# Kernel optimization log

Hardware: AMD Instinct MI355X
Metric: run time of the kernel (lower is better)

## Reference

```python
import jax, jax.numpy as jnp
import numpy as np

B, T, S, H, E = 4, 2048, 2048, 16, 64  # batch, q_len, kv_len, heads, head_dim


def setup_inputs() -> dict:
    key = jax.random.key(0)
    kq, kk, kv, kl, kw = jax.random.split(key, 5)
    query = jax.random.normal(kq, (B, T, H * E), dtype=jnp.float32)
    key_t = jax.random.normal(kk, (B, S, H * E), dtype=jnp.float32)
    value = jax.random.normal(kv, (B, S, H * E), dtype=jnp.float32)
    # valid lengths in [S//2, S] so every row has at least one attendable key
    lengths = jax.random.randint(kl, (B,), S // 2, S + 1)
    key_padding_mask = jnp.arange(S)[None, :] < lengths[:, None]  # (B, S) bool, True = keep
    W_out = jax.random.normal(kw, (H * E, E), dtype=jnp.float32) * 0.02
    b_out = jnp.zeros((E,), dtype=jnp.float32)
    return {"query": query, "key": key_t, "value": value,
            "key_padding_mask": key_padding_mask, "W_out": W_out, "b_out": b_out}


def reference(query, key, value, key_padding_mask, W_out, b_out):
    # (B, N, H*E) -> (B, H, N, E)
    q = query.reshape(B, T, H, E).transpose(0, 2, 1, 3)
    k = key.reshape(B, S, H, E).transpose(0, 2, 1, 3)
    v = value.reshape(B, S, H, E).transpose(0, 2, 1, 3)
    softmax_temp = 1.0 / np.sqrt(E).astype(np.float32)
    scores = jnp.einsum('bhte,bhse->bhts', q * softmax_temp, k)  # (B,H,T,S)
    neg_inf = jnp.finfo(scores.dtype).min
    scores = jnp.where(key_padding_mask[:, None, None, :], scores, neg_inf)
    attn = jax.nn.softmax(scores, axis=-1)  # dropout p=0 -> identity
    out = jnp.einsum('bhts,bhsd->bthd', attn, v)  # (B,T,H,E)
    out = out.reshape(B * T, H * E)
    return out @ W_out + b_out  # (B*T, E)
```

## Files before the change

### kernel.cpp

```cpp
#include <hip/hip_runtime.h>
#include <hip/hip_bf16.h>

#define Bq 4
#define Tq 2048
#define Sq 2048
#define Hq 16
#define Eq 64
#define HEq 1024

typedef __attribute__((ext_vector_type(8))) _Float16 half8;
typedef __attribute__((ext_vector_type(16))) float f32x16;

#define AS1 __attribute__((address_space(1)))
#define AS3 __attribute__((address_space(3)))

__device__ __forceinline__ void gl_lds16(const void* g, void* l) {
  __builtin_amdgcn_global_load_lds((const AS1 unsigned*)g, (AS3 unsigned*)l, 16, 0, 0);
}
#define VMCNT(n) asm volatile("s_waitcnt vmcnt(" #n ")" ::: "memory")
#define LGKM0 asm volatile("s_waitcnt lgkmcnt(0)" ::: "memory")

#if __has_builtin(__builtin_amdgcn_exp2f)
#define EXP2F(x) __builtin_amdgcn_exp2f(x)
#else
#define EXP2F(x) exp2f(x)
#endif

__device__ __forceinline__ unsigned pk16(float a, float b) {
  return __builtin_bit_cast(unsigned, __builtin_amdgcn_cvt_pkrtz(a, b));
}

__global__ __launch_bounds__(256) void prep_kernel(
    const float* __restrict__ K, const float* __restrict__ V,
    const float* __restrict__ W, const void* __restrict__ mask,
    _Float16* __restrict__ Kh, _Float16* __restrict__ VTh,
    _Float16* __restrict__ WT, int* __restrict__ lens) {
  __shared__ _Float16 tile[64][72];
  const int bid = blockIdx.x;
  const int tid = threadIdx.x;

  if (bid < 4096) {
    const size_t id = (size_t)bid * 256 + tid;
    const size_t o = id * 8;
    const int e0 = (int)(o & 63);
    const int s = (int)((o >> 6) & 2047);
    const int h = (int)((o >> 17) & 15);
    const int b = (int)(o >> 21);
    const float* src = K + ((size_t)(b * Sq + s) * HEq + h * Eq + e0);
    const float4 f0 = *(const float4*)src;
    const float4 f1 = *(const float4*)(src + 4);
    half8 hv;
    hv[0] = (_Float16)f0.x; hv[1] = (_Float16)f0.y;
    hv[2] = (_Float16)f0.z; hv[3] = (_Float16)f0.w;
    hv[4] = (_Float16)f1.x; hv[5] = (_Float16)f1.y;
    hv[6] = (_Float16)f1.z; hv[7] = (_Float16)f1.w;
    *(half8*)(Kh + o) = hv;
  } else if (bid < 6144) {
    const int b2 = bid - 4096;
    const int st = b2 & 31, h = (b2 >> 5) & 15, b = b2 >> 9;
    const int s0 = st * 64;
    const int s_in = tid >> 2, e0 = (tid & 3) * 16;
    const float* src = V + ((size_t)(b * Sq + s0 + s_in) * HEq + h * Eq + e0);
#pragma unroll
    for (int i = 0; i < 4; ++i) {
      const float4 f = *(const float4*)(src + i * 4);
      tile[s_in][e0 + i * 4 + 0] = (_Float16)f.x;
      tile[s_in][e0 + i * 4 + 1] = (_Float16)f.y;
      tile[s_in][e0 + i * 4 + 2] = (_Float16)f.z;
      tile[s_in][e0 + i * 4 + 3] = (_Float16)f.w;
    }
    __syncthreads();
    const int e_out = tid >> 2, sb = (tid & 3) * 16;
    half8 o0, o1;
#pragma unroll
    for (int j = 0; j < 8; ++j) {
      o0[j] = tile[sb + j][e_out];
      o1[j] = tile[sb + 8 + j][e_out];
    }
    _Float16* dst = VTh + ((size_t)((b * Hq + h) * Eq + e_out) * Sq + s0 + sb);
    *(half8*)dst = o0;
    *(half8*)(dst + 8) = o1;
  } else if (bid < 6400) {
    const int id = (bid - 6144) * 256 + tid;
    const int n = id >> 10, k = id & 1023;
    WT[id] = (_Float16)W[k * Eq + n];
  } else if (tid < 64) {
    const int b = bid - 6400;
    const int lane = tid;
    const unsigned w0 = *(const unsigned*)mask;
    int cnt = 0;
    if (w0 == 1u) {
      const int* m = (const int*)mask + b * Sq;
      for (int s = lane; s < Sq; s += 64) cnt += (m[s] != 0);
    } else if (w0 == 0x3F800000u) {
      const float* m = (const float*)mask + b * Sq;
      for (int s = lane; s < Sq; s += 64) cnt += (m[s] != 0.f);
    } else {
      const unsigned char* m = (const unsigned char*)mask + b * Sq;
      for (int s = lane; s < Sq; s += 64) cnt += (m[s] != 0);
    }
    for (int o = 32; o; o >>= 1) cnt += __shfl_down(cnt, o);
    if (lane == 0) lens[b] = cnt;
  }
}

__global__ __launch_bounds__(512, 4) void flash_kernel(
    const float* __restrict__ Q, const _Float16* __restrict__ Kh,
    const _Float16* __restrict__ VTh, const int* __restrict__ lens,
    _Float16* __restrict__ attnO) {
  __shared__ __align__(16) _Float16 KV[2][2][4096];

  const int bid = blockIdx.x;
  const int pair = bid & 63;
  const int qt = bid >> 6;
  const int h = pair & 15, b = pair >> 4;
  const int tid = threadIdx.x;
  const int w = tid >> 6, lane = tid & 63;
  const int qq = lane & 31, hi = lane >> 5;
  const int len = lens[b];
  const int q0 = qt * 256 + w * 32;

  const float qscale = 0.125f * 1.44269504088896340736f;
  half8 qf[4];
  {
    const float* qrow = Q + ((size_t)(b * Tq + q0 + qq) * HEq + h * Eq);
#pragma unroll
    for (int kw = 0; kw < 4; ++kw) {
      const float4 f0 = *(const float4*)(qrow + kw * 16 + hi * 8);
      const float4 f1 = *(const float4*)(qrow + kw * 16 + hi * 8 + 4);
      half8 qv;
      qv[0] = (_Float16)(f0.x * qscale);
      qv[1] = (_Float16)(f0.y * qscale);
      qv[2] = (_Float16)(f0.z * qscale);
      qv[3] = (_Float16)(f0.w * qscale);
      qv[4] = (_Float16)(f1.x * qscale);
      qv[5] = (_Float16)(f1.y * qscale);
      qv[6] = (_Float16)(f1.z * qscale);
      qv[7] = (_Float16)(f1.w * qscale);
      qf[kw] = qv;
    }
  }

  f32x16 Oa[2];
#pragma unroll
  for (int i = 0; i < 2; ++i)
#pragma unroll
    for (int r = 0; r < 16; ++r) Oa[i][r] = 0.f;
  float ls0 = 0.f, ls1 = 0.f;

  const char* kbase = (const char*)(Kh + (size_t)(b * Hq + h) * Sq * Eq);
  const char* vtbase = (const char*)(VTh + (size_t)(b * Hq + h) * Sq * Eq);

  const int row = w * 8 + (lane >> 3);
  const int colb = ((lane & 7) * 16) ^ (((lane >> 3) & 7) << 4);

  const int ntiles = (len + 63) >> 6;

  gl_lds16(kbase + (size_t)row * 128 + colb, (char*)&KV[0][0][0] + w * 1024);
  gl_lds16(vtbase + (size_t)row * 4096 + colb, (char*)&KV[0][1][0] + w * 1024);

  int p = 0;
  for (int t = 0; t < ntiles; ++t) {
    const int s0 = t << 6;
    if (t + 1 < ntiles) {
      const size_t kb = (size_t)(s0 + 64) * 128;
      const size_t vb = (size_t)(s0 + 64) * 2;
      gl_lds16(kbase + kb + (size_t)row * 128 + colb,
               (char*)&KV[p ^ 1][0][0] + w * 1024);
      gl_lds16(vtbase + vb + (size_t)row * 4096 + colb,
               (char*)&KV[p ^ 1][1][0] + w * 1024);
      VMCNT(2);
    } else {
      VMCNT(0);
    }
    __builtin_amdgcn_s_barrier();
    __builtin_amdgcn_sched_barrier(0);

    __builtin_amdgcn_s_setprio(1);
    f32x16 sc[2];
#pragma unroll
    for (int sm = 0; sm < 2; ++sm) {
      f32x16 acc;
#pragma unroll
      for (int r = 0; r < 16; ++r) acc[r] = 0.f;
#pragma unroll
      for (int kw = 0; kw < 4; ++kw) {
        const int arow = sm * 32 + qq;
        const half8 kf = *(const half8*)((const char*)&KV[p][0][0] + arow * 128 +
                                         ((kw * 32 + hi * 16) ^ ((arow & 7) << 4)));
        acc = __builtin_amdgcn_mfma_f32_32x32x16_f16(kf, qf[kw], acc, 0, 0, 0);
      }
      sc[sm] = acc;
    }
    __builtin_amdgcn_s_setprio(0);

    const int svalid = len - s0;
    if (svalid < 64) {
#pragma unroll
      for (int r = 0; r < 16; ++r) {
        const int sl = (r & 3) + 8 * (r >> 2) + 4 * hi;
        if (sl >= svalid) sc[0][r] = -60000.f;
        if (32 + sl >= svalid) sc[1][r] = -60000.f;
      }
    }

    unsigned pku[2][4][2];
#pragma unroll
    for (int sm = 0; sm < 2; ++sm)
#pragma unroll
      for (int rb = 0; rb < 4; ++rb)
#pragma unroll
        for (int pp = 0; pp < 2; ++pp) {
          const float a0 = EXP2F(sc[sm][rb * 4 + pp * 2]);
          const float a1 = EXP2F(sc[sm][rb * 4 + pp * 2 + 1]);
          ls0 += a0;
          ls1 += a1;
          pku[sm][rb][pp] = pk16(a0, a1);
        }

#pragma unroll
    for (int kw = 0; kw < 4; ++kw) {
      const int sm = kw >> 1;
      const int rbe = (kw & 1) * 2, rbo = rbe + 1;
      union { unsigned u[4]; half8 h; } pu;
#pragma unroll
      for (int pp = 0; pp < 2; ++pp) {
        const unsigned ev = pku[sm][rbe][pp];
        const unsigned od = pku[sm][rbo][pp];
        const unsigned sendv = hi ? ev : od;
        const unsigned recvv = __shfl_xor(sendv, 32);
        pu.u[pp] = hi ? recvv : ev;
        pu.u[2 + pp] = hi ? od : recvv;
      }
      const half8 pf = pu.h;
      __builtin_amdgcn_s_setprio(1);
#pragma unroll
      for (int eh = 0; eh < 2; ++eh) {
        const int vrow = eh * 32 + qq;
        const half8 vf = *(const half8*)((const char*)&KV[p][1][0] + vrow * 128 +
                                         ((kw * 32 + hi * 16) ^ ((vrow & 7) << 4)));
        Oa[eh] = __builtin_amdgcn_mfma_f32_32x32x16_f16(vf, pf, Oa[eh], 0, 0, 0);
      }
      __builtin_amdgcn_s_setprio(0);
    }

    __builtin_amdgcn_s_barrier();
    __builtin_amdgcn_sched_barrier(0);
    p ^= 1;
  }

  float ls = ls0 + ls1;
  ls += __shfl_xor(ls, 32);
  const float inv = 1.f / ls;
  char* const scratch = (char*)&KV[0][0][0] + w * 4096;
#pragma unroll
  for (int eh = 0; eh < 2; ++eh)
#pragma unroll
    for (int rb = 0; rb < 4; ++rb)
#pragma unroll
      for (int pp = 0; pp < 2; ++pp) {
        const int e0 = eh * 32 + rb * 8 + hi * 4 + pp * 2;
        const unsigned uo = pk16(Oa[eh][rb * 4 + pp * 2] * inv,
                                 Oa[eh][rb * 4 + pp * 2 + 1] * inv);
        *(unsigned*)(scratch + qq * 128 + ((e0 * 2) ^ ((qq & 7) << 4))) = uo;
      }
  LGKM0;
  __builtin_amdgcn_sched_barrier(0);
#pragma unroll
  for (int i = 0; i < 4; ++i) {
    const int qr = i * 8 + (lane >> 3), ch = lane & 7;
    const half8 ov = *(const half8*)(scratch + qr * 128 + ((ch * 16) ^ ((qr & 7) << 4)));
    *(half8*)(attnO + (size_t)(b * Tq + q0 + qr) * HEq + h * Eq + ch * 8) = ov;
  }
}

typedef __attribute__((ext_vector_type(4))) float floatx4;
__global__ __launch_bounds__(256) void proj_kernel(
    const _Float16* __restrict__ A, const _Float16* __restrict__ WT,
    const float* __restrict__ bias, float* __restrict__ out) {
  const int tid = threadIdx.x;
  const int w = tid >> 6, lane = tid & 63;
  const int g = lane >> 4, c = lane & 15;
  const int r0 = blockIdx.x * 64 + w * 16;
  floatx4 acc[4];
#pragma unroll
  for (int i = 0; i < 4; ++i) acc[i] = (floatx4){0.f, 0.f, 0.f, 0.f};
  const _Float16* arow = A + (size_t)(r0 + c) * HEq;
  for (int kc = 0; kc < 32; ++kc) {
    const half8 af = *(const half8*)(arow + kc * 32 + g * 8);
#pragma unroll
    for (int nt = 0; nt < 4; ++nt) {
      const half8 bf =
          *(const half8*)(WT + (size_t)(nt * 16 + c) * HEq + kc * 32 + g * 8);
      acc[nt] = __builtin_amdgcn_mfma_f32_16x16x32_f16(af, bf, acc[nt], 0, 0, 0);
    }
  }
#pragma unroll
  for (int r = 0; r < 4; ++r) {
    const int row = r0 + g * 4 + r;
#pragma unroll
    for (int nt = 0; nt < 4; ++nt) {
      const int col = nt * 16 + c;
      out[(size_t)row * Eq + col] = acc[nt][r] + bias[col];
    }
  }
}

extern "C" void kernel_launch(void* const* d_in, const int* in_sizes, int n_in,
                              void* d_out, int out_size, void* d_ws, size_t ws_size,
                              hipStream_t stream) {
  const float* q = (const float*)d_in[0];
  const float* k = (const float*)d_in[1];
  const float* v = (const float*)d_in[2];
  const void* mask = d_in[3];
  const float* W = (const float*)d_in[4];
  const float* bias = (const float*)d_in[5];
  float* out = (float*)d_out;

  char* ws = (char*)d_ws;
  int* lens = (int*)ws;
  _Float16* WT = (_Float16*)(ws + 256);
  _Float16* attn = (_Float16*)(ws + (256 + 131072));
  _Float16* Kh = (_Float16*)(ws + (256 + 131072 + (1 << 24)));
  _Float16* VTh = (_Float16*)(ws + (256 + 131072 + (1 << 24) + (1 << 24)));

  prep_kernel<<<6404, 256, 0, stream>>>(k, v, W, mask, Kh, VTh, WT, lens);
  flash_kernel<<<512, 512, 0, stream>>>(q, Kh, VTh, lens, attn);
  proj_kernel<<<(Bq * Tq) / 64, 256, 0, stream>>>(attn, WT, bias, out);
}
```

Baseline: 112.9 us.

## Pre-pack K and V into MFMA-fragment tile order for contiguous LDS loads

The prep kernel now converts K and V into per-64-row tiles stored already in the exact fragment order the flash kernel's MFMA reads use. K also goes through the shared-memory tile path, and the separate transposed V layout is replaced by a packed layout. The flash kernel then issues fully contiguous 16-byte global-to-LDS copies with no XOR swizzle, and its LDS reads are linear per lane. The aim is to simplify address math and make global loads perfectly coalesced, at the cost of a more complex prep step and possible LDS bank conflicts in the unswizzled reads.

Result: faster. 110.0 us (-2.6%).

```diff
diff --git a/kernel.cpp b/kernel.cpp
--- a/kernel.cpp
+++ b/kernel.cpp
@@ -33,34 +33,20 @@
 __global__ __launch_bounds__(256) void prep_kernel(
     const float* __restrict__ K, const float* __restrict__ V,
     const float* __restrict__ W, const void* __restrict__ mask,
-    _Float16* __restrict__ Kh, _Float16* __restrict__ VTh,
+    char* __restrict__ KP, char* __restrict__ VP,
     _Float16* __restrict__ WT, int* __restrict__ lens) {
   __shared__ _Float16 tile[64][72];
   const int bid = blockIdx.x;
   const int tid = threadIdx.x;
 
   if (bid < 4096) {
-    const size_t id = (size_t)bid * 256 + tid;
-    const size_t o = id * 8;
-    const int e0 = (int)(o & 63);
-    const int s = (int)((o >> 6) & 2047);
-    const int h = (int)((o >> 17) & 15);
-    const int b = (int)(o >> 21);
-    const float* src = K + ((size_t)(b * Sq + s) * HEq + h * Eq + e0);
-    const float4 f0 = *(const float4*)src;
-    const float4 f1 = *(const float4*)(src + 4);
-    half8 hv;
-    hv[0] = (_Float16)f0.x; hv[1] = (_Float16)f0.y;
-    hv[2] = (_Float16)f0.z; hv[3] = (_Float16)f0.w;
-    hv[4] = (_Float16)f1.x; hv[5] = (_Float16)f1.y;
-    hv[6] = (_Float16)f1.z; hv[7] = (_Float16)f1.w;
-    *(half8*)(Kh + o) = hv;
-  } else if (bid < 6144) {
-    const int b2 = bid - 4096;
-    const int st = b2 & 31, h = (b2 >> 5) & 15, b = b2 >> 9;
-    const int s0 = st * 64;
+    const int isV = bid >= 2048;
+    const int b2 = bid & 2047;
+    const int t = b2 & 31, h = (b2 >> 5) & 15, b = b2 >> 9;
+    const int s0 = t * 64;
     const int s_in = tid >> 2, e0 = (tid & 3) * 16;
-    const float* src = V + ((size_t)(b * Sq + s0 + s_in) * HEq + h * Eq + e0);
+    const float* X = isV ? V : K;
+    const float* src = X + ((size_t)(b * Sq + s0 + s_in) * HEq + h * Eq + e0);
 #pragma unroll
     for (int i = 0; i < 4; ++i) {
       const float4 f = *(const float4*)(src + i * 4);
@@ -70,22 +56,34 @@
       tile[s_in][e0 + i * 4 + 3] = (_Float16)f.w;
     }
     __syncthreads();
-    const int e_out = tid >> 2, sb = (tid & 3) * 16;
-    half8 o0, o1;
-#pragma unroll
-    for (int j = 0; j < 8; ++j) {
-      o0[j] = tile[sb + j][e_out];
-      o1[j] = tile[sb + 8 + j][e_out];
-    }
-    _Float16* dst = VTh + ((size_t)((b * Hq + h) * Eq + e_out) * Sq + s0 + sb);
-    *(half8*)dst = o0;
-    *(half8*)(dst + 8) = o1;
-  } else if (bid < 6400) {
-    const int id = (bid - 6144) * 256 + tid;
+    half8 u0, u1;
+    if (!isV) {
+      const int gi = tid >> 5, sl = (tid & 31) * 2;
+#pragma unroll
+      for (int j = 0; j < 8; ++j) {
+        u0[j] = tile[sl][gi * 8 + j];
+        u1[j] = tile[sl + 1][gi * 8 + j];
+      }
+      char* dst = KP + ((size_t)b2 * 8192) + tid * 32;
+      *(half8*)dst = u0;
+      *(half8*)(dst + 16) = u1;
+    } else {
+      const int sgi = tid >> 5, e = (tid & 31) * 2;
+#pragma unroll
+      for (int j = 0; j < 8; ++j) {
+        u0[j] = tile[sgi * 8 + j][e];
+        u1[j] = tile[sgi * 8 + j][e + 1];
+      }
+      char* dst = VP + ((size_t)b2 * 8192) + tid * 32;
+      *(half8*)dst = u0;
+      *(half8*)(dst + 16) = u1;
+    }
+  } else if (bid < 4352) {
+    const int id = (bid - 4096) * 256 + tid;
     const int n = id >> 10, k = id & 1023;
     WT[id] = (_Float16)W[k * Eq + n];
   } else if (tid < 64) {
-    const int b = bid - 6400;
+    const int b = bid - 4352;
     const int lane = tid;
     const unsigned w0 = *(const unsigned*)mask;
     int cnt = 0;
@@ -105,8 +103,8 @@
 }
 
 __global__ __launch_bounds__(512, 4) void flash_kernel(
-    const float* __restrict__ Q, const _Float16* __restrict__ Kh,
-    const _Float16* __restrict__ VTh, const int* __restrict__ lens,
+    const float* __restrict__ Q, const char* __restrict__ KP,
+    const char* __restrict__ VP, const int* __restrict__ lens,
     _Float16* __restrict__ attnO) {
   __shared__ __align__(16) _Float16 KV[2][2][4096];
 
@@ -148,27 +146,21 @@
     for (int r = 0; r < 16; ++r) Oa[i][r] = 0.f;
   float ls0 = 0.f, ls1 = 0.f;
 
-  const char* kbase = (const char*)(Kh + (size_t)(b * Hq + h) * Sq * Eq);
-  const char* vtbase = (const char*)(VTh + (size_t)(b * Hq + h) * Sq * Eq);
-
-  const int row = w * 8 + (lane >> 3);
-  const int colb = ((lane & 7) * 16) ^ (((lane >> 3) & 7) << 4);
+  const char* kpb = KP + (size_t)(b * Hq + h) * 32 * 8192;
+  const char* vpb = VP + (size_t)(b * Hq + h) * 32 * 8192;
+  const int so = w * 1024 + lane * 16;
 
   const int ntiles = (len + 63) >> 6;
 
-  gl_lds16(kbase + (size_t)row * 128 + colb, (char*)&KV[0][0][0] + w * 1024);
-  gl_lds16(vtbase + (size_t)row * 4096 + colb, (char*)&KV[0][1][0] + w * 1024);
+  gl_lds16(kpb + so, (char*)&KV[0][0][0] + so);
+  gl_lds16(vpb + so, (char*)&KV[0][1][0] + so);
 
   int p = 0;
   for (int t = 0; t < ntiles; ++t) {
-    const int s0 = t << 6;
     if (t + 1 < ntiles) {
-      const size_t kb = (size_t)(s0 + 64) * 128;
-      const size_t vb = (size_t)(s0 + 64) * 2;
-      gl_lds16(kbase + kb + (size_t)row * 128 + colb,
-               (char*)&KV[p ^ 1][0][0] + w * 1024);
-      gl_lds16(vtbase + vb + (size_t)row * 4096 + colb,
-               (char*)&KV[p ^ 1][1][0] + w * 1024);
+      const size_t tb = (size_t)(t + 1) * 8192;
+      gl_lds16(kpb + tb + so, (char*)&KV[p ^ 1][0][0] + so);
+      gl_lds16(vpb + tb + so, (char*)&KV[p ^ 1][1][0] + so);
       VMCNT(2);
     } else {
       VMCNT(0);
@@ -185,16 +177,15 @@
       for (int r = 0; r < 16; ++r) acc[r] = 0.f;
 #pragma unroll
       for (int kw = 0; kw < 4; ++kw) {
-        const int arow = sm * 32 + qq;
-        const half8 kf = *(const half8*)((const char*)&KV[p][0][0] + arow * 128 +
-                                         ((kw * 32 + hi * 16) ^ ((arow & 7) << 4)));
+        const half8 kf = *(const half8*)((const char*)&KV[p][0][0] +
+                                         (kw * 2 + hi) * 1024 + (sm * 32 + qq) * 16);
         acc = __builtin_amdgcn_mfma_f32_32x32x16_f16(kf, qf[kw], acc, 0, 0, 0);
       }
       sc[sm] = acc;
     }
     __builtin_amdgcn_s_setprio(0);
 
-    const int svalid = len - s0;
+    const int svalid = len - (t << 6);
     if (svalid < 64) {
 #pragma unroll
       for (int r = 0; r < 16; ++r) {
@@ -236,9 +227,8 @@
       __builtin_amdgcn_s_setprio(1);
 #pragma unroll
       for (int eh = 0; eh < 2; ++eh) {
-        const int vrow = eh * 32 + qq;
-        const half8 vf = *(const half8*)((const char*)&KV[p][1][0] + vrow * 128 +
-                                         ((kw * 32 + hi * 16) ^ ((vrow & 7) << 4)));
+        const half8 vf = *(const half8*)((const char*)&KV[p][1][0] +
+                                         (kw * 2 + hi) * 1024 + (eh * 32 + qq) * 16);
         Oa[eh] = __builtin_amdgcn_mfma_f32_32x32x16_f16(vf, pf, Oa[eh], 0, 0, 0);
       }
       __builtin_amdgcn_s_setprio(0);
@@ -321,10 +311,10 @@
   int* lens = (int*)ws;
   _Float16* WT = (_Float16*)(ws + 256);
   _Float16* attn = (_Float16*)(ws + (256 + 131072));
-  _Float16* Kh = (_Float16*)(ws + (256 + 131072 + (1 << 24)));
-  _Float16* VTh = (_Float16*)(ws + (256 + 131072 + (1 << 24) + (1 << 24)));
-
-  prep_kernel<<<6404, 256, 0, stream>>>(k, v, W, mask, Kh, VTh, WT, lens);
-  flash_kernel<<<512, 512, 0, stream>>>(q, Kh, VTh, lens, attn);
+  char* KP = ws + (256 + 131072 + (1 << 24));
+  char* VP = ws + (256 + 131072 + (1 << 24) + (1 << 24));
+
+  prep_kernel<<<4356, 256, 0, stream>>>(k, v, W, mask, KP, VP, WT, lens);
+  flash_kernel<<<512, 512, 0, stream>>>(q, KP, VP, lens, attn);
   proj_kernel<<<(Bq * Tq) / 64, 256, 0, stream>>>(attn, WT, bias, out);
 }
```
